# Optimization experiments

Measured on AMD Instinct MI355X. Metric: run time of the kernel, lower is better.

## Reference

```python
import jax, jax.numpy as jnp
import numpy as np

B = 1
T, H, W = 8, 20, 20
N = T * H * W  # 3200
DIM = 3072
NH = 24
HD = DIM // NH  # 128
D_T, D_H, D_W = 32, 48, 48  # 3D RoPE split of head_dim
EPS = 1e-6


def _axis_freqs(d, n):
    # [n, d//2] angles for one axis
    inv = 1.0 / (10000.0 ** (jnp.arange(0, d, 2, dtype=jnp.float32) / d))
    return jnp.arange(n, dtype=jnp.float32)[:, None] * inv[None, :]


def rope3d_cos_sin(t, h, w):
    ft = jnp.broadcast_to(_axis_freqs(D_T, t)[:, None, None, :], (t, h, w, D_T // 2))
    fh = jnp.broadcast_to(_axis_freqs(D_H, h)[None, :, None, :], (t, h, w, D_H // 2))
    fw = jnp.broadcast_to(_axis_freqs(D_W, w)[None, None, :, :], (t, h, w, D_W // 2))
    f = jnp.concatenate([ft, fh, fw], axis=-1).reshape(t * h * w, HD // 2)
    return jnp.cos(f), jnp.sin(f)


def apply_rope(x, cos, sin):
    # x: [B, N, NH, HD]; interleaved pairs rotation
    xf = x.astype(jnp.float32).reshape(*x.shape[:-1], HD // 2, 2)
    x1, x2 = xf[..., 0], xf[..., 1]
    c = cos[None, :, None, :]
    s = sin[None, :, None, :]
    r1 = x1 * c - x2 * s
    r2 = x1 * s + x2 * c
    return jnp.stack([r1, r2], axis=-1).reshape(x.shape).astype(x.dtype)


def rmsnorm(x, w):
    xf = x.astype(jnp.float32)
    n = xf * jax.lax.rsqrt(jnp.mean(xf * xf, axis=-1, keepdims=True) + EPS)
    return (n * w).astype(x.dtype)


def setup_inputs() -> dict:
    key = jax.random.key(0)
    ks = jax.random.split(key, 6)
    scale = 0.02
    return {
        "x": jax.random.normal(ks[0], (B, N, DIM), jnp.float32),
        "Wq": jax.random.normal(ks[1], (DIM, DIM), jnp.float32) * scale,
        "bq": jnp.zeros((DIM,), jnp.float32),
        "Wk": jax.random.normal(ks[2], (DIM, DIM), jnp.float32) * scale,
        "bk": jnp.zeros((DIM,), jnp.float32),
        "Wv": jax.random.normal(ks[3], (DIM, DIM), jnp.float32) * scale,
        "bv": jnp.zeros((DIM,), jnp.float32),
        "Wo": jax.random.normal(ks[4], (DIM, DIM), jnp.float32) * scale,
        "bo": jnp.zeros((DIM,), jnp.float32),
        "q_norm_w": jnp.ones((HD,), jnp.float32),
        "k_norm_w": jnp.ones((HD,), jnp.float32),
        "num_cond_latents": 2,
    }


def reference(x, Wq, bq, Wk, bk, Wv, bv, Wo, bo, q_norm_w, k_norm_w, num_cond_latents):
    # QKV projections -> [B, N, NH, HD]
    q = (x @ Wq + bq).reshape(B, N, NH, HD)
    k = (x @ Wk + bk).reshape(B, N, NH, HD)
    v = (x @ Wv + bv).reshape(B, N, NH, HD)
    # per-head RMSNorm on q, k
    q = rmsnorm(q, q_norm_w)
    k = rmsnorm(k, k_norm_w)
    # 3D RoPE over (T, H, W) grid
    cos, sin = rope3d_cos_sin(T, H, W)
    q = apply_rope(q, cos, sin)
    k = apply_rope(k, cos, sin)
    # I2V split: cond tokens attend only to themselves; noise tokens attend to all
    nct = num_cond_latents * (N // T)  # static python int
    out_cond = jax.nn.dot_product_attention(q[:, :nct], k[:, :nct], v[:, :nct])
    out_noise = jax.nn.dot_product_attention(q[:, nct:], k, v)
    out = jnp.concatenate([out_cond, out_noise], axis=1).reshape(B, N, DIM)
    return out @ Wo + bo
```

## Files before the change

kernel.cpp:

```cpp
#include <hip/hip_runtime.h>
#include <stdint.h>

typedef _Float16 f16;
typedef _Float16 f16x2 __attribute__((ext_vector_type(2)));
typedef _Float16 f16x4 __attribute__((ext_vector_type(4)));
typedef _Float16 f16x8 __attribute__((ext_vector_type(8)));
typedef float f32x4 __attribute__((ext_vector_type(4)));
typedef float f32x16 __attribute__((ext_vector_type(16)));

#define DIM   3072
#define NTOK  3200
#define NHEAD 24
#define SCALE 0.08838834764831845f

__device__ __forceinline__ void async16(const void* g, void* l) {
  __builtin_amdgcn_global_load_lds(
      (const __attribute__((address_space(1))) uint32_t*)g,
      (__attribute__((address_space(3))) uint32_t*)l, 16, 0, 0);
}

__device__ __forceinline__ uint32_t pkrtz(float a, float b) {
  auto p = __builtin_amdgcn_cvt_pkrtz(a, b);
  return __builtin_bit_cast(uint32_t, p);
}

__device__ __forceinline__ f32x4 mfma16(f16x8 a, f16x8 b, f32x4 c) {
  return __builtin_amdgcn_mfma_f32_16x16x32_f16(a, b, c, 0, 0, 0);
}


__global__ __launch_bounds__(256) void cvt_f32_f16(const float* __restrict__ in,
                                                   f16* __restrict__ out) {
  size_t i = ((size_t)blockIdx.x * 256 + threadIdx.x) * 4;
  float4 v = *(const float4*)(in + i);
  f16x4 o = {(f16)v.x, (f16)v.y, (f16)v.z, (f16)v.w};
  *(f16x4*)(out + i) = o;
}

__global__ __launch_bounds__(256) void transpose4(
    const float* __restrict__ W0, const float* __restrict__ W1,
    const float* __restrict__ W2, const float* __restrict__ W3,
    f16* __restrict__ T0, f16* __restrict__ T1,
    f16* __restrict__ T2, f16* __restrict__ T3) {
  const float* W; f16* T;
  switch (blockIdx.z) {
    case 0: W = W0; T = T0; break;
    case 1: W = W1; T = T1; break;
    case 2: W = W2; T = T2; break;
    default: W = W3; T = T3; break;
  }
  __shared__ float t[32][33];
  int tx = threadIdx.x & 31, ty = threadIdx.x >> 5;
  size_t bx = (size_t)blockIdx.x * 32, by = (size_t)blockIdx.y * 32;
#pragma unroll
  for (int r = 0; r < 4; ++r)
    t[ty + r * 8][tx] = W[(by + ty + r * 8) * DIM + bx + tx];
  __syncthreads();
#pragma unroll
  for (int r = 0; r < 4; ++r)
    T[(bx + ty + r * 8) * DIM + by + tx] = (f16)t[tx][ty + r * 8];
}

__global__ __launch_bounds__(256) void rope_tables(float* __restrict__ cosT,
                                                   float* __restrict__ sinT) {
  int tid = blockIdx.x * 256 + threadIdx.x;
  int p = tid >> 6, j = tid & 63;
  int t = p / 400, rem = p % 400;
  int hh = rem / 20, ww = rem % 20;
  float val, e;
  if (j < 16)      { val = (float)t;  e = (float)(2 * j)        * (1.f / 32.f); }
  else if (j < 40) { val = (float)hh; e = (float)(2 * (j - 16)) * (1.f / 48.f); }
  else             { val = (float)ww; e = (float)(2 * (j - 40)) * (1.f / 48.f); }
  float f = val * expf(-e * 9.210340371976184f);
  cosT[tid] = cosf(f);
  sinT[tid] = sinf(f);
}


__device__ __forceinline__ void stage_half(const f16* __restrict__ base, int row0,
                                           int rowmax, int k0, char* ldsdst, int tid) {
#pragma unroll
  for (int s = 0; s < 2; ++s) {
    int idx = s * 512 + tid;
    int r = idx >> 3, pc = idx & 7;
    int cc = pc ^ (r & 7);
    int grow = row0 + r;
    grow = grow < rowmax ? grow : rowmax - 1;
    async16(base + (size_t)grow * DIM + k0 + cc * 8, ldsdst + idx * 16);
  }
}

__device__ __forceinline__ void gemm256_body(
    const f16* __restrict__ A, const f16* __restrict__ Bm,
    const float* __restrict__ bias, void* __restrict__ C,
    int m0, int n0, int Mrows, int mode, char* smem) {

  const int tid = threadIdx.x;
  const int lane = tid & 63, w = tid >> 6;
  const int wm = w >> 2, wn = w & 3;
  const int l15 = lane & 15, l4 = lane >> 4;

  f32x4 acc[8][4];
#pragma unroll
  for (int m = 0; m < 8; ++m)
#pragma unroll
    for (int n = 0; n < 4; ++n) acc[m][n] = (f32x4){0.f, 0.f, 0.f, 0.f};

  const int NT = DIM / 64;

  stage_half(A,  m0,       Mrows,   0,  smem + 0,     tid);
  stage_half(Bm, n0,       1 << 30, 0,  smem + 32768, tid);
  stage_half(A,  m0 + 128, Mrows,   0,  smem + 16384, tid);
  stage_half(Bm, n0 + 128, 1 << 30, 0,  smem + 49152, tid);
  stage_half(A,  m0,       Mrows,   64, smem + 65536, tid);
  asm volatile("s_waitcnt vmcnt(2)" ::: "memory");
  __builtin_amdgcn_s_barrier();

  const int arow0 = wm * 128 + l15;
  const int brow0 = wn * 64 + l15;

  for (int t = 0; t < NT; ++t) {
    char* bufc = smem + (t & 1) * 65536;
    char* bufn = smem + ((t + 1) & 1) * 65536;
    const f16* Ald = (const f16*)bufc;
    const f16* Bld = (const f16*)(bufc + 32768);
    int k1 = (t + 1) * 64; k1 = k1 <= DIM - 64 ? k1 : DIM - 64;
    int k2 = (t + 2) * 64; k2 = k2 <= DIM - 64 ? k2 : DIM - 64;

    f16x8 af[8], b0, b1;

#pragma unroll
    for (int m = 0; m < 8; ++m) {
      int r = arow0 + m * 16, pc = l4 ^ (r & 7);
      af[m] = *(const f16x8*)(Ald + r * 64 + pc * 8);
    }
    { int r = brow0,      pc = l4 ^ (r & 7); b0 = *(const f16x8*)(Bld + r * 64 + pc * 8);
      r = brow0 + 16;     pc = l4 ^ (r & 7); b1 = *(const f16x8*)(Bld + r * 64 + pc * 8); }
    stage_half(Bm, n0, 1 << 30, k1, bufn + 32768, tid);
    __builtin_amdgcn_s_barrier();
    asm volatile("s_waitcnt lgkmcnt(0)" ::: "memory");
    __builtin_amdgcn_sched_barrier(0);
    __builtin_amdgcn_s_setprio(1);
#pragma unroll
    for (int m = 0; m < 8; ++m) {
      acc[m][0] = mfma16(af[m], b0, acc[m][0]);
      acc[m][1] = mfma16(af[m], b1, acc[m][1]);
    }
    __builtin_amdgcn_s_setprio(0);
    __builtin_amdgcn_s_barrier();

    { int r = brow0 + 32, pc = l4 ^ (r & 7); b0 = *(const f16x8*)(Bld + r * 64 + pc * 8);
      r = brow0 + 48;     pc = l4 ^ (r & 7); b1 = *(const f16x8*)(Bld + r * 64 + pc * 8); }
    stage_half(A, m0 + 128, Mrows, k1, bufn + 16384, tid);
    __builtin_amdgcn_s_barrier();
    asm volatile("s_waitcnt lgkmcnt(0)" ::: "memory");
    __builtin_amdgcn_sched_barrier(0);
    __builtin_amdgcn_s_setprio(1);
#pragma unroll
    for (int m = 0; m < 8; ++m) {
      acc[m][2] = mfma16(af[m], b0, acc[m][2]);
      acc[m][3] = mfma16(af[m], b1, acc[m][3]);
    }
    __builtin_amdgcn_s_setprio(0);
    __builtin_amdgcn_s_barrier();

#pragma unroll
    for (int m = 0; m < 8; ++m) {
      int r = arow0 + m * 16, pc = (4 + l4) ^ (r & 7);
      af[m] = *(const f16x8*)(Ald + r * 64 + pc * 8);
    }
    { int r = brow0,      pc = (4 + l4) ^ (r & 7); b0 = *(const f16x8*)(Bld + r * 64 + pc * 8);
      r = brow0 + 16;     pc = (4 + l4) ^ (r & 7); b1 = *(const f16x8*)(Bld + r * 64 + pc * 8); }
    stage_half(Bm, n0 + 128, 1 << 30, k1, bufn + 49152, tid);
    __builtin_amdgcn_s_barrier();
    asm volatile("s_waitcnt lgkmcnt(0)" ::: "memory");
    __builtin_amdgcn_sched_barrier(0);
    __builtin_amdgcn_s_setprio(1);
#pragma unroll
    for (int m = 0; m < 8; ++m) {
      acc[m][0] = mfma16(af[m], b0, acc[m][0]);
      acc[m][1] = mfma16(af[m], b1, acc[m][1]);
    }
    __builtin_amdgcn_s_setprio(0);
    __builtin_amdgcn_s_barrier();

    { int r = brow0 + 32, pc = (4 + l4) ^ (r & 7); b0 = *(const f16x8*)(Bld + r * 64 + pc * 8);
      r = brow0 + 48;     pc = (4 + l4) ^ (r & 7); b1 = *(const f16x8*)(Bld + r * 64 + pc * 8); }
    stage_half(A, m0, Mrows, k2, bufc + 0, tid);
    __builtin_amdgcn_s_barrier();
    asm volatile("s_waitcnt lgkmcnt(0)" ::: "memory");
    __builtin_amdgcn_sched_barrier(0);
    __builtin_amdgcn_s_setprio(1);
#pragma unroll
    for (int m = 0; m < 8; ++m) {
      acc[m][2] = mfma16(af[m], b0, acc[m][2]);
      acc[m][3] = mfma16(af[m], b1, acc[m][3]);
    }
    __builtin_amdgcn_s_setprio(0);
    asm volatile("s_waitcnt vmcnt(2)" ::: "memory");
    __builtin_amdgcn_s_barrier();
  }

#pragma unroll
  for (int n = 0; n < 4; ++n) {
    int col = n0 + wn * 64 + n * 16 + l15;
    float bb = bias[col];
#pragma unroll
    for (int m = 0; m < 8; ++m) {
      int rbase = m0 + wm * 128 + m * 16 + l4 * 4;
      if (rbase < Mrows) {
        if (mode == 2) {
          f16x4 ov;
#pragma unroll
          for (int r = 0; r < 4; ++r) ov[r] = (f16)(acc[m][n][r] + bb);
          *(f16x4*)((f16*)C + (size_t)col * NTOK + rbase) = ov;
        } else if (mode == 1) {
#pragma unroll
          for (int r = 0; r < 4; ++r)
            ((float*)C)[(size_t)(rbase + r) * DIM + col] = acc[m][n][r] + bb;
        } else {
#pragma unroll
          for (int r = 0; r < 4; ++r)
            ((f16*)C)[(size_t)(rbase + r) * DIM + col] = (f16)(acc[m][n][r] + bb);
        }
      }
    }
  }
}

__global__ __launch_bounds__(512, 2) void gemm256_qkv(
    const f16* __restrict__ A,
    const f16* __restrict__ B0, const f16* __restrict__ B1, const f16* __restrict__ B2,
    const float* __restrict__ b0, const float* __restrict__ b1, const float* __restrict__ b2,
    f16* __restrict__ C0, f16* __restrict__ C1, f16* __restrict__ C2) {
  __shared__ char smem[131072];
  int sel = blockIdx.y / 12, yn = blockIdx.y % 12;
  const f16* B = sel == 0 ? B0 : (sel == 1 ? B1 : B2);
  const float* bias = sel == 0 ? b0 : (sel == 1 ? b1 : b2);
  f16* C = sel == 0 ? C0 : (sel == 1 ? C1 : C2);
  gemm256_body(A, B, bias, C, blockIdx.x * 256, yn * 256, NTOK, sel == 2 ? 2 : 0, smem);
}

__global__ __launch_bounds__(512, 2) void gemm256_out(
    const f16* __restrict__ A, const f16* __restrict__ B,
    const float* __restrict__ bias, float* __restrict__ C) {
  __shared__ char smem[131072];
  gemm256_body(A, B, bias, C, blockIdx.x * 256, blockIdx.y * 256, NTOK, 1, smem);
}

__global__ __launch_bounds__(256) void rmsnorm_rope(
    f16* __restrict__ qk, const float* __restrict__ w,
    const float* __restrict__ cosT, const float* __restrict__ sinT, float osc) {
  int lane = threadIdx.x & 63, rb = threadIdx.x >> 6;
  int row = blockIdx.x * 4 + rb;
  int p = row / NHEAD;
  f16* ptr = qk + (size_t)row * 128 + lane * 2;
  f16x2 hv = *(const f16x2*)ptr;
  float x1 = (float)hv[0], x2 = (float)hv[1];
  float ss = x1 * x1 + x2 * x2;
#pragma unroll
  for (int o = 32; o > 0; o >>= 1) ss += __shfl_xor(ss, o);
  float r = rsqrtf(ss * (1.f / 128.f) + 1e-6f);
  float n1 = x1 * r * w[lane * 2], n2 = x2 * r * w[lane * 2 + 1];
  float c = cosT[p * 64 + lane], s = sinT[p * 64 + lane];
  f16x2 ov = {(f16)((n1 * c - n2 * s) * osc), (f16)((n1 * s + n2 * c) * osc)};
  *(f16x2*)ptr = ov;
}

__global__ __launch_bounds__(320) void attn2(
    const f16* __restrict__ q, const f16* __restrict__ k, const f16* __restrict__ vt,
    f16* __restrict__ out) {
  extern __shared__ char smem[];
  f16* Ks = (f16*)smem;
  f16* Vs = (f16*)(smem + 32768);

  int L = blockIdx.x;
  int c = L & 7, j = L >> 3;
  int head = c * 3 + j / 20, qblk = j % 20;
  int q0 = qblk * 160;
  int kv_len = (q0 < 800) ? 800 : 3200;

  const int tid = threadIdx.x, lane = tid & 63, w = tid >> 6;
  const int l31 = lane & 31, hi = lane >> 5;
  const int qg = q0 + w * 32 + l31;
  const int sw_base = l31 & 15;

  f16x8 qr[8];
#pragma unroll
  for (int ks = 0; ks < 8; ++ks)
    qr[ks] = *(const f16x8*)(q + (size_t)qg * DIM + head * 128 + ks * 16 + hi * 8);

  f32x16 o[4];
#pragma unroll
  for (int mb = 0; mb < 4; ++mb)
#pragma unroll
    for (int r = 0; r < 16; ++r) o[mb][r] = 0.f;
  float m_run = -1e30f, l_run = 0.f;

  for (int t0 = 0; t0 < kv_len; t0 += 128) {
    __syncthreads();
#pragma unroll
    for (int r = 0; r < 13; ++r) {
      int idx = r * 320 + tid;
      if (idx < 4096) {
        int row = (idx >> 4) & 127;
        int sw = (idx & 15) ^ (row & 15);
        const f16* src;
        if (idx < 2048) src = k + (size_t)(t0 + row) * DIM + head * 128 + sw * 8;
        else            src = vt + ((size_t)head * 128 + row) * NTOK + t0 + sw * 8;
        async16(src, (char*)(idx < 2048 ? Ks : Vs) + (idx & 2047) * 16);
      }
    }
    __syncthreads();

    const int nvb = min(4, (kv_len - t0) >> 5);

    f32x16 s4[4];
#pragma unroll
    for (int b = 0; b < 4; ++b)
#pragma unroll
      for (int r = 0; r < 16; ++r) s4[b][r] = 0.f;
#pragma unroll
    for (int ks = 0; ks < 8; ++ks) {
#pragma unroll
      for (int b = 0; b < 4; ++b) {
        if (b < nvb) {
          const f16x8 kf = *(const f16x8*)(Ks + ((b * 32 + l31) << 7) +
                                           (((ks * 2 + hi) ^ sw_base) << 3));
          s4[b] = __builtin_amdgcn_mfma_f32_32x32x16_f16(kf, qr[ks], s4[b], 0, 0, 0);
        }
      }
    }

    float tmax = -1e30f;
#pragma unroll
    for (int b = 0; b < 4; ++b)
      if (b < nvb)
#pragma unroll
        for (int r = 0; r < 16; ++r) tmax = fmaxf(tmax, s4[b][r]);
    tmax = fmaxf(tmax, __shfl_xor(tmax, 32));
    if (!__all(tmax <= m_run + 8.f)) {
      float mn = fmaxf(m_run, tmax);
      float alpha = __expf(m_run - mn);
      l_run *= alpha;
#pragma unroll
      for (int mb = 0; mb < 4; ++mb)
#pragma unroll
        for (int r = 0; r < 16; ++r) o[mb][r] *= alpha;
      m_run = mn;
    }
    float rs = 0.f;
#pragma unroll
    for (int b = 0; b < 4; ++b)
      if (b < nvb)
#pragma unroll
        for (int r = 0; r < 16; ++r) {
          float e = __expf(s4[b][r] - m_run);
          s4[b][r] = e;
          rs += e;
        }
    l_run += rs;

    const int nks = nvb * 2;
#pragma unroll
    for (int ks = 0; ks < 8; ++ks) {
      if (ks < nks) {
        const int b = ks >> 1, s8 = (ks & 1) * 8;
        uint32_t a0 = pkrtz(s4[b][s8 + 0], s4[b][s8 + 1]);
        uint32_t b0 = pkrtz(s4[b][s8 + 4], s4[b][s8 + 5]);
        asm("v_permlane32_swap_b32 %0, %1" : "+v"(a0), "+v"(b0));
        uint32_t a1 = pkrtz(s4[b][s8 + 2], s4[b][s8 + 3]);
        uint32_t b1 = pkrtz(s4[b][s8 + 6], s4[b][s8 + 7]);
        asm("v_permlane32_swap_b32 %0, %1" : "+v"(a1), "+v"(b1));
        union { uint32_t u[4]; f16x8 v; } pf;
        pf.u[0] = a0; pf.u[1] = a1; pf.u[2] = b0; pf.u[3] = b1;
#pragma unroll
        for (int mb = 0; mb < 4; ++mb) {
          const f16x8 vf = *(const f16x8*)(Vs + ((mb * 32 + l31) << 7) +
                                           (((ks * 2 + hi) ^ sw_base) << 3));
          o[mb] = __builtin_amdgcn_mfma_f32_32x32x16_f16(vf, pf.v, o[mb], 0, 0, 0);
        }
      }
    }
  }

  l_run += __shfl_xor(l_run, 32);
  float inv = 1.f / l_run;
#pragma unroll
  for (int mb = 0; mb < 4; ++mb)
#pragma unroll
    for (int jq = 0; jq < 4; ++jq) {
      f16x4 ov;
#pragma unroll
      for (int e = 0; e < 4; ++e) ov[e] = (f16)(o[mb][jq * 4 + e] * inv);
      *(f16x4*)(out + (size_t)qg * DIM + head * 128 + mb * 32 + jq * 8 + hi * 4) = ov;
    }
}


extern "C" void kernel_launch(void* const* d_in, const int* in_sizes, int n_in,
                              void* d_out, int out_size, void* d_ws, size_t ws_size,
                              hipStream_t stream) {
  const float* x   = (const float*)d_in[0];
  const float* Wq  = (const float*)d_in[1];
  const float* bq  = (const float*)d_in[2];
  const float* Wk  = (const float*)d_in[3];
  const float* bk  = (const float*)d_in[4];
  const float* Wv  = (const float*)d_in[5];
  const float* bv  = (const float*)d_in[6];
  const float* Wo  = (const float*)d_in[7];
  const float* bo  = (const float*)d_in[8];
  const float* qnw = (const float*)d_in[9];
  const float* knw = (const float*)d_in[10];

  char* ws = (char*)d_ws;
  f16*   xb   = (f16*)(ws);
  f16*   WqT  = (f16*)(ws + 19660800);
  f16*   WkT  = (f16*)(ws + 38535168);
  f16*   WvT  = (f16*)(ws + 57409536);
  f16*   WoT  = (f16*)(ws + 76283904);
  f16*   qb   = (f16*)(ws + 95158272);
  f16*   kb   = (f16*)(ws + 114819072);
  f16*   vtb  = (f16*)(ws + 134479872);
  f16*   ab   = (f16*)(ws + 154140672);
  float* cosT = (float*)(ws + 173801472);
  float* sinT = (float*)(ws + 174620672);

  cvt_f32_f16<<<9600, 256, 0, stream>>>(x, xb);
  transpose4<<<dim3(96, 96, 4), 256, 0, stream>>>(Wq, Wk, Wv, Wo, WqT, WkT, WvT, WoT);
  rope_tables<<<800, 256, 0, stream>>>(cosT, sinT);

  gemm256_qkv<<<dim3(13, 36), 512, 0, stream>>>(xb, WqT, WkT, WvT, bq, bk, bv, qb, kb, vtb);

  rmsnorm_rope<<<19200, 256, 0, stream>>>(qb, qnw, cosT, sinT, SCALE);
  rmsnorm_rope<<<19200, 256, 0, stream>>>(kb, knw, cosT, sinT, 1.0f);

  attn2<<<480, 320, 65536, stream>>>(qb, kb, vtb, ab);

  gemm256_out<<<dim3(13, 12), 512, 0, stream>>>(ab, WoT, bo, (float*)d_out);
}
```

Measured before the change: 559.1 us.

## Split K/V loads in attention to prefetch next K tile during PV

The attention kernel now loads K and V in separate phases. The V tile load overlaps the QK^T MFMAs, and the next K tile is prefetched while the PV MFMAs run, which removes the fully serialized load-then-compute step per tile. The log2(e) factor is folded into the q scale so softmax can use exp2f, with the rescale threshold adjusted to match. s_setprio is raised around the MFMA blocks. The price is an extra barrier per iteration and a more delicate ordering of async LDS writes against reads.

```diff
diff --git a/kernel.cpp b/kernel.cpp
--- a/kernel.cpp
+++ b/kernel.cpp
@@ -12,6 +12,7 @@
 #define NTOK  3200
 #define NHEAD 24
 #define SCALE 0.08838834764831845f
+#define LOG2E 1.4426950408889634f
 
 __device__ __forceinline__ void async16(const void* g, void* l) {
   __builtin_amdgcn_global_load_lds(
@@ -267,10 +268,10 @@
   *(f16x2*)ptr = ov;
 }
 
-__global__ __launch_bounds__(320) void attn2(
+__global__ __launch_bounds__(320) void attn3(
     const f16* __restrict__ q, const f16* __restrict__ k, const f16* __restrict__ vt,
     f16* __restrict__ out) {
-  extern __shared__ char smem[];
+  __shared__ char smem[65536];
   f16* Ks = (f16*)smem;
   f16* Vs = (f16*)(smem + 32768);
 
@@ -297,21 +298,28 @@
     for (int r = 0; r < 16; ++r) o[mb][r] = 0.f;
   float m_run = -1e30f, l_run = 0.f;
 
+#pragma unroll
+  for (int r = 0; r < 7; ++r) {
+    int idx = r * 320 + tid;
+    if (idx < 2048) {
+      int row = idx >> 4;
+      int sw = (idx & 15) ^ (row & 15);
+      async16(k + (size_t)row * DIM + head * 128 + sw * 8, (char*)Ks + idx * 16);
+    }
+  }
+  __syncthreads();
+
   for (int t0 = 0; t0 < kv_len; t0 += 128) {
-    __syncthreads();
-#pragma unroll
-    for (int r = 0; r < 13; ++r) {
+#pragma unroll
+    for (int r = 0; r < 7; ++r) {
       int idx = r * 320 + tid;
-      if (idx < 4096) {
-        int row = (idx >> 4) & 127;
+      if (idx < 2048) {
+        int row = idx >> 4;
         int sw = (idx & 15) ^ (row & 15);
-        const f16* src;
-        if (idx < 2048) src = k + (size_t)(t0 + row) * DIM + head * 128 + sw * 8;
-        else            src = vt + ((size_t)head * 128 + row) * NTOK + t0 + sw * 8;
-        async16(src, (char*)(idx < 2048 ? Ks : Vs) + (idx & 2047) * 16);
+        async16(vt + ((size_t)head * 128 + row) * NTOK + t0 + sw * 8,
+                (char*)Vs + idx * 16);
       }
     }
-    __syncthreads();
 
     const int nvb = min(4, (kv_len - t0) >> 5);
 
@@ -320,6 +328,7 @@
     for (int b = 0; b < 4; ++b)
 #pragma unroll
       for (int r = 0; r < 16; ++r) s4[b][r] = 0.f;
+    __builtin_amdgcn_s_setprio(1);
 #pragma unroll
     for (int ks = 0; ks < 8; ++ks) {
 #pragma unroll
@@ -331,6 +340,7 @@
         }
       }
     }
+    __builtin_amdgcn_s_setprio(0);
 
     float tmax = -1e30f;
 #pragma unroll
@@ -339,9 +349,9 @@
 #pragma unroll
         for (int r = 0; r < 16; ++r) tmax = fmaxf(tmax, s4[b][r]);
     tmax = fmaxf(tmax, __shfl_xor(tmax, 32));
-    if (!__all(tmax <= m_run + 8.f)) {
+    if (!__all(tmax <= m_run + 11.54f)) {
       float mn = fmaxf(m_run, tmax);
-      float alpha = __expf(m_run - mn);
+      float alpha = exp2f(m_run - mn);
       l_run *= alpha;
 #pragma unroll
       for (int mb = 0; mb < 4; ++mb)
@@ -355,11 +365,26 @@
       if (b < nvb)
 #pragma unroll
         for (int r = 0; r < 16; ++r) {
-          float e = __expf(s4[b][r] - m_run);
+          float e = exp2f(s4[b][r] - m_run);
           s4[b][r] = e;
           rs += e;
         }
     l_run += rs;
+
+    __syncthreads();
+
+    if (t0 + 128 < kv_len) {
+#pragma unroll
+      for (int r = 0; r < 7; ++r) {
+        int idx = r * 320 + tid;
+        if (idx < 2048) {
+          int row = idx >> 4;
+          int sw = (idx & 15) ^ (row & 15);
+          async16(k + (size_t)(t0 + 128 + row) * DIM + head * 128 + sw * 8,
+                  (char*)Ks + idx * 16);
+        }
+      }
+    }
 
     const int nks = nvb * 2;
 #pragma unroll
@@ -374,14 +399,18 @@
         asm("v_permlane32_swap_b32 %0, %1" : "+v"(a1), "+v"(b1));
         union { uint32_t u[4]; f16x8 v; } pf;
         pf.u[0] = a0; pf.u[1] = a1; pf.u[2] = b0; pf.u[3] = b1;
+        __builtin_amdgcn_s_setprio(1);
 #pragma unroll
         for (int mb = 0; mb < 4; ++mb) {
           const f16x8 vf = *(const f16x8*)(Vs + ((mb * 32 + l31) << 7) +
                                            (((ks * 2 + hi) ^ sw_base) << 3));
           o[mb] = __builtin_amdgcn_mfma_f32_32x32x16_f16(vf, pf.v, o[mb], 0, 0, 0);
         }
+        __builtin_amdgcn_s_setprio(0);
       }
     }
+
+    __syncthreads();
   }
 
   l_run += __shfl_xor(l_run, 32);
@@ -432,10 +461,10 @@
 
   gemm256_qkv<<<dim3(13, 36), 512, 0, stream>>>(xb, WqT, WkT, WvT, bq, bk, bv, qb, kb, vtb);
 
-  rmsnorm_rope<<<19200, 256, 0, stream>>>(qb, qnw, cosT, sinT, SCALE);
+  rmsnorm_rope<<<19200, 256, 0, stream>>>(qb, qnw, cosT, sinT, SCALE * LOG2E);
   rmsnorm_rope<<<19200, 256, 0, stream>>>(kb, knw, cosT, sinT, 1.0f);
 
-  attn2<<<480, 320, 65536, stream>>>(qb, kb, vtb, ab);
+  attn3<<<480, 320, 0, stream>>>(qb, kb, vtb, ab);
 
   gemm256_out<<<dim3(13, 12), 512, 0, stream>>>(ab, WoT, bo, (float*)d_out);
 }
```

Measured after the change: 585.8 us. +4.8%, slower.

## Use exp2 softmax with folded log2e, MFMA row sums, setprio, fused q/k norm

Applied to the files above, without the earlier changes.

The attention softmax now works in base 2: log2(e) is folded into the q scale during RMSNorm/RoPE, and raw v_exp_f32 replaces __expf, with the rescale threshold adjusted to match. Row sums of P are computed by an extra MFMA against a ones vector instead of per-lane scalar adds, which also removes the final cross-half shuffle. MFMA sections are wrapped in s_setprio, and the two rmsnorm_rope launches are merged into one 2D grid. LDS becomes static, and the async-copy address math is simplified. The extra MFMA adds matrix-unit work per tile in exchange for fewer VALU adds.

```diff
diff --git a/kernel.cpp b/kernel.cpp
--- a/kernel.cpp
+++ b/kernel.cpp
@@ -12,6 +12,7 @@
 #define NTOK  3200
 #define NHEAD 24
 #define SCALE 0.08838834764831845f
+#define LOG2E 1.4426950408889634f
 
 __device__ __forceinline__ void async16(const void* g, void* l) {
   __builtin_amdgcn_global_load_lds(
@@ -22,6 +23,12 @@
 __device__ __forceinline__ uint32_t pkrtz(float a, float b) {
   auto p = __builtin_amdgcn_cvt_pkrtz(a, b);
   return __builtin_bit_cast(uint32_t, p);
+}
+
+__device__ __forceinline__ float fexp2(float x) {
+  float r;
+  asm("v_exp_f32 %0, %1" : "=v"(r) : "v"(x));
+  return r;
 }
 
 __device__ __forceinline__ f32x4 mfma16(f16x8 a, f16x8 b, f32x4 c) {
@@ -248,9 +255,13 @@
   gemm256_body(A, B, bias, C, blockIdx.x * 256, blockIdx.y * 256, NTOK, 1, smem);
 }
 
-__global__ __launch_bounds__(256) void rmsnorm_rope(
-    f16* __restrict__ qk, const float* __restrict__ w,
-    const float* __restrict__ cosT, const float* __restrict__ sinT, float osc) {
+__global__ __launch_bounds__(256) void rmsnorm_rope2(
+    f16* __restrict__ qbuf, f16* __restrict__ kbuf,
+    const float* __restrict__ qw, const float* __restrict__ kw,
+    const float* __restrict__ cosT, const float* __restrict__ sinT) {
+  f16* qk = blockIdx.y ? kbuf : qbuf;
+  const float* w = blockIdx.y ? kw : qw;
+  const float osc = blockIdx.y ? 1.0f : SCALE * LOG2E;
   int lane = threadIdx.x & 63, rb = threadIdx.x >> 6;
   int row = blockIdx.x * 4 + rb;
   int p = row / NHEAD;
@@ -267,10 +278,10 @@
   *(f16x2*)ptr = ov;
 }
 
-__global__ __launch_bounds__(320) void attn2(
+__global__ __launch_bounds__(320) void attn5(
     const f16* __restrict__ q, const f16* __restrict__ k, const f16* __restrict__ vt,
     f16* __restrict__ out) {
-  extern __shared__ char smem[];
+  __shared__ char smem[65536];
   f16* Ks = (f16*)smem;
   f16* Vs = (f16*)(smem + 32768);
 
@@ -290,12 +301,16 @@
   for (int ks = 0; ks < 8; ++ks)
     qr[ks] = *(const f16x8*)(q + (size_t)qg * DIM + head * 128 + ks * 16 + hi * 8);
 
-  f32x16 o[4];
+  const f16x8 ones = {(f16)1, (f16)1, (f16)1, (f16)1, (f16)1, (f16)1, (f16)1, (f16)1};
+
+  f32x16 o[4], lsum;
 #pragma unroll
   for (int mb = 0; mb < 4; ++mb)
 #pragma unroll
     for (int r = 0; r < 16; ++r) o[mb][r] = 0.f;
-  float m_run = -1e30f, l_run = 0.f;
+#pragma unroll
+  for (int r = 0; r < 16; ++r) lsum[r] = 0.f;
+  float m_run = -1e30f;
 
   for (int t0 = 0; t0 < kv_len; t0 += 128) {
     __syncthreads();
@@ -308,7 +323,7 @@
         const f16* src;
         if (idx < 2048) src = k + (size_t)(t0 + row) * DIM + head * 128 + sw * 8;
         else            src = vt + ((size_t)head * 128 + row) * NTOK + t0 + sw * 8;
-        async16(src, (char*)(idx < 2048 ? Ks : Vs) + (idx & 2047) * 16);
+        async16(src, smem + idx * 16);
       }
     }
     __syncthreads();
@@ -320,6 +335,7 @@
     for (int b = 0; b < 4; ++b)
 #pragma unroll
       for (int r = 0; r < 16; ++r) s4[b][r] = 0.f;
+    __builtin_amdgcn_s_setprio(1);
 #pragma unroll
     for (int ks = 0; ks < 8; ++ks) {
 #pragma unroll
@@ -331,35 +347,33 @@
         }
       }
     }
+    __builtin_amdgcn_s_setprio(0);
 
     float tmax = -1e30f;
 #pragma unroll
     for (int b = 0; b < 4; ++b)
       if (b < nvb)
 #pragma unroll
-        for (int r = 0; r < 16; ++r) tmax = fmaxf(tmax, s4[b][r]);
+        for (int r = 0; r < 16; r += 2)
+          tmax = fmaxf(tmax, fmaxf(s4[b][r], s4[b][r + 1]));
     tmax = fmaxf(tmax, __shfl_xor(tmax, 32));
-    if (!__all(tmax <= m_run + 8.f)) {
+    if (!__all(tmax <= m_run + 11.54f)) {
       float mn = fmaxf(m_run, tmax);
-      float alpha = __expf(m_run - mn);
-      l_run *= alpha;
+      float alpha = fexp2(m_run - mn);
 #pragma unroll
       for (int mb = 0; mb < 4; ++mb)
 #pragma unroll
         for (int r = 0; r < 16; ++r) o[mb][r] *= alpha;
+#pragma unroll
+      for (int r = 0; r < 16; ++r) lsum[r] *= alpha;
       m_run = mn;
     }
-    float rs = 0.f;
 #pragma unroll
     for (int b = 0; b < 4; ++b)
       if (b < nvb)
 #pragma unroll
-        for (int r = 0; r < 16; ++r) {
-          float e = __expf(s4[b][r] - m_run);
-          s4[b][r] = e;
-          rs += e;
-        }
-    l_run += rs;
+        for (int r = 0; r < 16; ++r)
+          s4[b][r] = fexp2(s4[b][r] - m_run);
 
     const int nks = nvb * 2;
 #pragma unroll
@@ -374,18 +388,20 @@
         asm("v_permlane32_swap_b32 %0, %1" : "+v"(a1), "+v"(b1));
         union { uint32_t u[4]; f16x8 v; } pf;
         pf.u[0] = a0; pf.u[1] = a1; pf.u[2] = b0; pf.u[3] = b1;
+        __builtin_amdgcn_s_setprio(1);
 #pragma unroll
         for (int mb = 0; mb < 4; ++mb) {
           const f16x8 vf = *(const f16x8*)(Vs + ((mb * 32 + l31) << 7) +
                                            (((ks * 2 + hi) ^ sw_base) << 3));
           o[mb] = __builtin_amdgcn_mfma_f32_32x32x16_f16(vf, pf.v, o[mb], 0, 0, 0);
         }
+        lsum = __builtin_amdgcn_mfma_f32_32x32x16_f16(ones, pf.v, lsum, 0, 0, 0);
+        __builtin_amdgcn_s_setprio(0);
       }
     }
   }
 
-  l_run += __shfl_xor(l_run, 32);
-  float inv = 1.f / l_run;
+  float inv = 1.f / lsum[0];
 #pragma unroll
   for (int mb = 0; mb < 4; ++mb)
 #pragma unroll
@@ -432,10 +448,9 @@
 
   gemm256_qkv<<<dim3(13, 36), 512, 0, stream>>>(xb, WqT, WkT, WvT, bq, bk, bv, qb, kb, vtb);
 
-  rmsnorm_rope<<<19200, 256, 0, stream>>>(qb, qnw, cosT, sinT, SCALE);
-  rmsnorm_rope<<<19200, 256, 0, stream>>>(kb, knw, cosT, sinT, 1.0f);
-
-  attn2<<<480, 320, 65536, stream>>>(qb, kb, vtb, ab);
+  rmsnorm_rope2<<<dim3(19200, 2), 256, 0, stream>>>(qb, kb, qnw, knw, cosT, sinT);
+
+  attn5<<<480, 320, 0, stream>>>(qb, kb, vtb, ab);
 
   gemm256_out<<<dim3(13, 12), 512, 0, stream>>>(ab, WoT, bo, (float*)d_out);
 }
```

New measurement: 568.8 us. No clear change (+1.7%).
